# Kernel optimization log

Hardware: AMD Instinct MI355X
Metric: run time of the kernel (lower is better)

Reference implementation:

```python
import jax, jax.numpy as jnp
import numpy as np

DIM = 1024
DEPTH = 2
D_STATE = 16
EXPAND = 2            # standard Mamba expand factor -> d_inner = 2*dim
D_CONV = 4
DT_RANK = DIM // 16   # ceil(dim/16) = 64
D_INNER = DIM * EXPAND
BATCH = 2
SEQ = 1024


def setup_inputs() -> dict:
    key = jax.random.key(0)
    ks = jax.random.split(key, 8)
    def n(k, shape, scale):
        return jax.random.normal(k, shape, jnp.float32) * scale
    # A_log initialized as log(1..N) per channel (S4D-real init, as in mamba_ssm)
    A_log = jnp.tile(jnp.log(jnp.arange(1, D_STATE + 1, dtype=jnp.float32))[None, None, :],
                     (DEPTH, D_INNER, 1))
    return {
        "x": n(ks[0], (BATCH, SEQ, DIM), 1.0),
        "in_proj_w": n(ks[1], (DEPTH, 2 * D_INNER, DIM), DIM ** -0.5),
        "conv_w": n(ks[2], (DEPTH, D_INNER, D_CONV), D_CONV ** -0.5),
        "conv_b": jnp.zeros((DEPTH, D_INNER), jnp.float32),
        "x_proj_w": n(ks[3], (DEPTH, DT_RANK + 2 * D_STATE, D_INNER), D_INNER ** -0.5),
        "dt_proj_w": n(ks[4], (DEPTH, D_INNER, DT_RANK), DT_RANK ** -0.5),
        "dt_proj_b": n(ks[5], (DEPTH, D_INNER), 0.1),
        "A_log": A_log,
        "D": jnp.ones((DEPTH, D_INNER), jnp.float32),
        "out_proj_w": n(ks[6], (DEPTH, DIM, D_INNER), D_INNER ** -0.5),
    }


def _mamba_layer(x, in_w, cw, cb, xp_w, dtw, dtb, A_log, Dp, ow):
    # x: [B, L, dim]
    Bsz = x.shape[0]
    xz = jnp.einsum('bld,ed->ble', x, in_w)            # [B, L, 2*d_inner]
    xi, z = jnp.split(xz, 2, axis=-1)
    # causal depthwise conv1d over time
    xc = jnp.transpose(xi, (0, 2, 1))                  # [B, d_inner, L]
    xc = jax.lax.conv_general_dilated(xc, cw[:, None, :], (1,), [(D_CONV - 1, 0)],
                                      feature_group_count=D_INNER)
    xc = xc + cb[None, :, None]
    xc = jax.nn.silu(jnp.transpose(xc, (0, 2, 1)))     # [B, L, d_inner]
    # input-dependent dt, B, C
    x_dbl = jnp.einsum('bld,ed->ble', xc, xp_w)        # [B, L, dt_rank+2*N]
    dt_raw = x_dbl[..., :DT_RANK]
    Bm = x_dbl[..., DT_RANK:DT_RANK + D_STATE]         # [B, L, N]
    Cm = x_dbl[..., DT_RANK + D_STATE:]                # [B, L, N]
    dt = jax.nn.softplus(jnp.einsum('blr,dr->bld', dt_raw, dtw) + dtb)  # [B, L, d_inner]
    A = -jnp.exp(A_log)                                # [d_inner, N]
    dA = jnp.exp(dt[..., None] * A[None, None])        # [B, L, d_inner, N]
    dBu = dt[..., None] * Bm[:, :, None, :] * xc[..., None]

    def step(h, inp):
        dA_t, dBu_t, C_t = inp
        h = dA_t * h + dBu_t                           # [B, d_inner, N]
        y = jnp.einsum('bdn,bn->bd', h, C_t)
        return h, y

    h0 = jnp.zeros((Bsz, D_INNER, D_STATE), x.dtype)
    _, ys = jax.lax.scan(step, h0,
                         (dA.transpose(1, 0, 2, 3), dBu.transpose(1, 0, 2, 3),
                          Cm.transpose(1, 0, 2)))
    y = ys.transpose(1, 0, 2) + Dp[None, None, :] * xc
    y = y * jax.nn.silu(z)
    return jnp.einsum('bld,od->blo', y, ow)


def reference(x, in_proj_w, conv_w, conv_b, x_proj_w, dt_proj_w, dt_proj_b, A_log, D, out_proj_w):
    for i in range(DEPTH):
        x = _mamba_layer(x, in_proj_w[i], conv_w[i], conv_b[i], x_proj_w[i],
                         dt_proj_w[i], dt_proj_b[i], A_log[i], D[i], out_proj_w[i])
    return x
```

## Files before the change

### kernel.cpp

```cpp
#include <hip/hip_runtime.h>
#include <hip/hip_bf16.h>

typedef __hip_bfloat16 bf16;
typedef __attribute__((ext_vector_type(8))) short short8;
typedef __attribute__((ext_vector_type(4))) short shortx4;
typedef __attribute__((ext_vector_type(4))) float floatx4;

#define BATCH   2
#define SEQ     1024
#define DIM     1024
#define D_INNER 2048
#define D_STATE 16
#define DT_RANK 64
#define MROWS   (BATCH * SEQ)
#define CHUNK   32
#define NCHUNK  (SEQ / CHUNK)

__device__ __forceinline__ float bf2f(bf16 x) { return __bfloat162float(x); }
__device__ __forceinline__ bf16  f2bf(float x) { return __float2bfloat16(x); }
__device__ __forceinline__ short bfbits(float x) {
    bf16 b = __float2bfloat16(x); short s; __builtin_memcpy(&s, &b, 2); return s;
}

__device__ __forceinline__ void ld_lds16(const void* g, void* l) {
    __builtin_amdgcn_global_load_lds(
        (const __attribute__((address_space(1))) void*)g,
        (__attribute__((address_space(3))) void*)l, 16, 0, 0);
}

__device__ __forceinline__ void cast4(const float* in, short* o, int i) {
    floatx4 v = ((const floatx4*)in)[i];
    shortx4 r;
    r.x = bfbits(v.x); r.y = bfbits(v.y); r.z = bfbits(v.z); r.w = bfbits(v.w);
    ((shortx4*)o)[i] = r;
}
__global__ __launch_bounds__(256) void cast_k(
    const float* __restrict__ in, short* __restrict__ o, int n4)
{
    int i = blockIdx.x * 256 + threadIdx.x;
    if (i < n4) cast4(in, o, i);
}
__global__ __launch_bounds__(256) void cast2_k(
    const float* __restrict__ a, short* __restrict__ oa, int na4,
    const float* __restrict__ b, short* __restrict__ ob, int nb4)
{
    int i = blockIdx.x * 256 + threadIdx.x;
    if (i < na4) cast4(a, oa, i);
    else if (i - na4 < nb4) cast4(b, ob, i - na4);
}

__device__ __forceinline__ short8 ld8_any(const void* p, size_t eoff, int is_f32) {
    if (is_f32) {
        const float* f = (const float*)p + eoff;
        floatx4 a = *(const floatx4*)f;
        floatx4 b = *(const floatx4*)(f + 4);
        short8 r;
        r[0] = bfbits(a[0]); r[1] = bfbits(a[1]); r[2] = bfbits(a[2]); r[3] = bfbits(a[3]);
        r[4] = bfbits(b[0]); r[5] = bfbits(b[1]); r[6] = bfbits(b[2]); r[7] = bfbits(b[3]);
        return r;
    } else {
        return *(const short8*)((const bf16*)p + eoff);
    }
}

__global__ __launch_bounds__(256) void gemm128(
    const bf16* __restrict__ A, int lda,
    const bf16* __restrict__ B, int ldb,
    float* __restrict__ Cf, bf16* __restrict__ Cb, int ldc,
    int kchunk, size_t psize)
{
    __shared__ short As[4][128 * 32];
    __shared__ short Bs[4][128 * 32];
    const int tid  = threadIdx.x;
    const int wave = tid >> 6;
    const int lane = tid & 63;
    const int m0 = blockIdx.y * 128;
    const int n0 = blockIdx.x * 128;
    const int wm = (wave & 1) * 64;
    const int wn = (wave >> 1) * 64;
    const int r16  = lane & 15;
    const int quad = lane >> 4;
    const int r0   = tid >> 2;
    const int csw   = (((tid & 3) ^ ((r0 >> 1) & 3)) << 3);
    const int swoff = ((quad ^ ((r16 >> 1) & 3)) << 3);
    const int kbeg = blockIdx.z * kchunk;
    const int nk   = kchunk >> 5;

    floatx4 acc[4][4] = {};

    auto STAGE = [&](int buf, int kk) {
        ld_lds16(A + (size_t)(m0 + r0) * lda + kk + csw,      &As[buf][tid * 8]);
        ld_lds16(A + (size_t)(m0 + r0 + 64) * lda + kk + csw, &As[buf][(tid + 256) * 8]);
        ld_lds16(B + (size_t)(n0 + r0) * ldb + kk + csw,      &Bs[buf][tid * 8]);
        ld_lds16(B + (size_t)(n0 + r0 + 64) * ldb + kk + csw, &Bs[buf][(tid + 256) * 8]);
    };
    auto COMPUTE = [&](int buf) {
        const short* Ab = As[buf];
        const short* Bb = Bs[buf];
        short8 af[4], bg[4];
#pragma unroll
        for (int i = 0; i < 4; i++) {
            af[i] = *(const short8*)(Ab + (wm + i * 16 + r16) * 32 + swoff);
            bg[i] = *(const short8*)(Bb + (wn + i * 16 + r16) * 32 + swoff);
        }
        __builtin_amdgcn_s_setprio(1);
#pragma unroll
        for (int i = 0; i < 4; i++)
#pragma unroll
            for (int j = 0; j < 4; j++)
                acc[i][j] = __builtin_amdgcn_mfma_f32_16x16x32_bf16(af[i], bg[j], acc[i][j], 0, 0, 0);
        __builtin_amdgcn_s_setprio(0);
    };

    STAGE(0, kbeg);
    STAGE(1, kbeg + 32);
    int it = 0;
    for (; it < nk - 2; ++it) {
        STAGE((it + 2) & 3, kbeg + (it + 2) * 32);
        asm volatile("s_waitcnt vmcnt(8) lgkmcnt(0)" ::: "memory");
        __builtin_amdgcn_s_barrier();
        __builtin_amdgcn_sched_barrier(0);
        COMPUTE(it & 3);
    }
    asm volatile("s_waitcnt vmcnt(4) lgkmcnt(0)" ::: "memory");
    __builtin_amdgcn_s_barrier();
    __builtin_amdgcn_sched_barrier(0);
    COMPUTE(it & 3);
    ++it;
    asm volatile("s_waitcnt vmcnt(0) lgkmcnt(0)" ::: "memory");
    __builtin_amdgcn_s_barrier();
    __builtin_amdgcn_sched_barrier(0);
    COMPUTE(it & 3);

    float* Cfp = Cf ? Cf + (size_t)blockIdx.z * psize : nullptr;
#pragma unroll
    for (int i = 0; i < 4; i++)
#pragma unroll
        for (int j = 0; j < 4; j++) {
            int gm = m0 + wm + i * 16 + quad * 4;
            int gn = n0 + wn + j * 16 + r16;
#pragma unroll
            for (int r = 0; r < 4; r++) {
                size_t o = (size_t)(gm + r) * ldc + gn;
                float v = acc[i][j][r];
                if (Cfp) Cfp[o] = v;
                if (Cb) Cb[o] = f2bf(v);
            }
        }
}

__global__ __launch_bounds__(256) void gemm_bt(
    const void* __restrict__ A, int a_f32, int lda,
    const void* __restrict__ B, int b_f32, int ldb,
    float* __restrict__ Cf, bf16* __restrict__ Cb, int ldc,
    int N, int K, size_t psize,
    const float* __restrict__ bias, int act)
{
    __shared__ short As[64][40];
    __shared__ short Bs[64][40];
    const int m0   = blockIdx.y * 64;
    const int n0   = blockIdx.x * 64;
    const int tid  = threadIdx.x;
    const int wave = tid >> 6;
    const int lane = tid & 63;
    const int srow = tid >> 2;
    const int scol = (tid & 3) << 3;
    const int r16  = lane & 15;
    const int quad = lane >> 4;
    const int kbeg = blockIdx.z * K;

    floatx4 acc[4] = {};

    for (int k0 = kbeg; k0 < kbeg + K; k0 += 32) {
        short8 av = ld8_any(A, (size_t)(m0 + srow) * lda + k0 + scol, a_f32);
        short8 bv = {};
        int gn = n0 + srow;
        if (gn < N) bv = ld8_any(B, (size_t)gn * ldb + k0 + scol, b_f32);
        *(short8*)(&As[srow][scol]) = av;
        *(short8*)(&Bs[srow][scol]) = bv;
        __syncthreads();
        short8 af = *(const short8*)(&As[wave * 16 + r16][quad * 8]);
#pragma unroll
        for (int nt = 0; nt < 4; nt++) {
            short8 bq = *(const short8*)(&Bs[nt * 16 + r16][quad * 8]);
            acc[nt] = __builtin_amdgcn_mfma_f32_16x16x32_bf16(af, bq, acc[nt], 0, 0, 0);
        }
        __syncthreads();
    }

    float* Cfp = Cf ? Cf + (size_t)blockIdx.z * psize : nullptr;
#pragma unroll
    for (int nt = 0; nt < 4; nt++) {
        int gn = n0 + nt * 16 + r16;
        if (gn >= N) continue;
        float bsv = bias ? bias[gn] : 0.f;
#pragma unroll
        for (int r = 0; r < 4; r++) {
            int gm = m0 + wave * 16 + quad * 4 + r;
            float v = acc[nt][r] + bsv;
            if (act == 1) v = (v > 20.f) ? v : log1pf(__expf(v));
            size_t o = (size_t)gm * ldc + gn;
            if (Cfp) Cfp[o] = v;
            if (Cb) Cb[o] = f2bf(v);
        }
    }
}

__global__ __launch_bounds__(256) void reduceN_k(
    const float* __restrict__ part, size_t psize, int n, int np,
    float* __restrict__ of, bf16* __restrict__ ob)
{
    int i = blockIdx.x * 256 + threadIdx.x;
    if (i >= n) return;
    float v = 0.f;
    for (int j = 0; j < np; j++) v += part[i + (size_t)j * psize];
    if (of) of[i] = v;
    if (ob) ob[i] = f2bf(v);
}

__global__ __launch_bounds__(256) void conv_silu_k(
    const bf16* __restrict__ xz, const float* __restrict__ cw,
    const float* __restrict__ cb, bf16* __restrict__ xcb)
{
    int idx = blockIdx.x * 256 + threadIdx.x;
    int d   = idx & (D_INNER - 1);
    int bt  = idx >> 11;
    int t   = bt & (SEQ - 1);
    float s = cb[d];
#pragma unroll
    for (int j = 0; j < 4; j++) {
        int tt = t - 3 + j;
        if (tt >= 0) s += cw[d * 4 + j] * bf2f(xz[(size_t)(bt - 3 + j) * 4096 + d]);
    }
    float sig = 1.f / (1.f + __expf(-s));
    xcb[idx] = f2bf(s * sig);
}

__global__ __launch_bounds__(256) void scan1_k(
    const float* __restrict__ dtf, const bf16* __restrict__ xcb,
    const float* __restrict__ xdbl, const float* __restrict__ Alog,
    float* __restrict__ chunk_sdt, float* __restrict__ chunk_S)
{
    __shared__ float dt_s[CHUNK][256];
    __shared__ short xc_s[CHUNK][256];
    __shared__ float B_s[CHUNK][16];
    const int tid = threadIdx.x;
    const int d0  = blockIdx.x * 256;
    const int d   = d0 + tid;
    const int b   = blockIdx.y;
    const int c   = blockIdx.z;
    const size_t rbase = (size_t)b * SEQ + c * CHUNK;

#pragma unroll 4
    for (int t = 0; t < CHUNK; t++) {
        dt_s[t][tid] = dtf[(rbase + t) * D_INNER + d0 + tid];
        ((short*)xc_s)[t * 256 + tid] = *(const short*)&xcb[(rbase + t) * D_INNER + d0 + tid];
    }
    for (int e = tid; e < CHUNK * 16; e += 256) {
        int t = e >> 4, n = e & 15;
        B_s[t][n] = xdbl[(rbase + t) * 96 + 64 + n];
    }
    float A[16];
#pragma unroll
    for (int n = 0; n < 16; n++) A[n] = -__expf(Alog[(size_t)d * 16 + n]);
    float h[16] = {};
    float sdt = 0.f;
    __syncthreads();

    for (int t = 0; t < CHUNK; t++) {
        float dtv = dt_s[t][tid];
        bf16 xcr; short xs = xc_s[t][tid]; __builtin_memcpy(&xcr, &xs, 2);
        float u = dtv * bf2f(xcr);
        sdt += dtv;
        floatx4 B0 = *(const floatx4*)&B_s[t][0];
        floatx4 B1 = *(const floatx4*)&B_s[t][4];
        floatx4 B2 = *(const floatx4*)&B_s[t][8];
        floatx4 B3 = *(const floatx4*)&B_s[t][12];
#pragma unroll
        for (int n = 0; n < 4; n++) {
            h[n]      = __expf(dtv * A[n])      * h[n]      + u * B0[n];
            h[n + 4]  = __expf(dtv * A[n + 4])  * h[n + 4]  + u * B1[n];
            h[n + 8]  = __expf(dtv * A[n + 8])  * h[n + 8]  + u * B2[n];
            h[n + 12] = __expf(dtv * A[n + 12]) * h[n + 12] + u * B3[n];
        }
    }
    chunk_sdt[(b * NCHUNK + c) * D_INNER + d] = sdt;
#pragma unroll
    for (int n = 0; n < 16; n++)
        chunk_S[((size_t)(b * NCHUNK + c) * 16 + n) * D_INNER + d] = h[n];
}

__global__ __launch_bounds__(256) void scanpre_k(
    const float* __restrict__ Alog, const float* __restrict__ chunk_sdt,
    float* __restrict__ chunk_S)
{
    const int d = blockIdx.x * 256 + threadIdx.x;
    const int b = blockIdx.y;
    const int n = blockIdx.z;
    const float Av = -__expf(Alog[(size_t)d * 16 + n]);
    float h = 0.f;
    for (int j = 0; j < NCHUNK; j++) {
        size_t si = ((size_t)(b * NCHUNK + j) * 16 + n) * D_INNER + d;
        float S   = chunk_S[si];
        float sdt = chunk_sdt[(b * NCHUNK + j) * D_INNER + d];
        chunk_S[si] = h;
        h = __expf(sdt * Av) * h + S;
    }
}

__global__ __launch_bounds__(256) void scan2_k(
    const float* __restrict__ dtf, const bf16* __restrict__ xcb,
    const float* __restrict__ xdbl, const bf16* __restrict__ xz,
    const float* __restrict__ Alog, const float* __restrict__ Dp,
    const float* __restrict__ chunk_S, bf16* __restrict__ yb)
{
    __shared__ float dt_s[CHUNK][256];
    __shared__ short xc_s[CHUNK][256];
    __shared__ float B_s[CHUNK][16];
    __shared__ float C_s[CHUNK][16];
    const int tid = threadIdx.x;
    const int d0  = blockIdx.x * 256;
    const int d   = d0 + tid;
    const int b   = blockIdx.y;
    const int c   = blockIdx.z;
    const size_t rbase = (size_t)b * SEQ + c * CHUNK;

#pragma unroll 4
    for (int t = 0; t < CHUNK; t++) {
        dt_s[t][tid] = dtf[(rbase + t) * D_INNER + d0 + tid];
        ((short*)xc_s)[t * 256 + tid] = *(const short*)&xcb[(rbase + t) * D_INNER + d0 + tid];
    }
    for (int e = tid; e < CHUNK * 16; e += 256) {
        int t = e >> 4, n = e & 15;
        B_s[t][n] = xdbl[(rbase + t) * 96 + 64 + n];
        C_s[t][n] = xdbl[(rbase + t) * 96 + 80 + n];
    }
    float A[16];
#pragma unroll
    for (int n = 0; n < 16; n++) A[n] = -__expf(Alog[(size_t)d * 16 + n]);

    float h[16];
#pragma unroll
    for (int n = 0; n < 16; n++)
        h[n] = chunk_S[((size_t)(b * NCHUNK + c) * 16 + n) * D_INNER + d];

    const float Dv = Dp[d];
    __syncthreads();

    for (int t = 0; t < CHUNK; t++) {
        size_t row = rbase + t;
        float dtv = dt_s[t][tid];
        bf16 xcr; short xs = xc_s[t][tid]; __builtin_memcpy(&xcr, &xs, 2);
        float xcv = bf2f(xcr);
        float u = dtv * xcv;
        floatx4 B0 = *(const floatx4*)&B_s[t][0];
        floatx4 B1 = *(const floatx4*)&B_s[t][4];
        floatx4 B2 = *(const floatx4*)&B_s[t][8];
        floatx4 B3 = *(const floatx4*)&B_s[t][12];
        floatx4 C0 = *(const floatx4*)&C_s[t][0];
        floatx4 C1 = *(const floatx4*)&C_s[t][4];
        floatx4 C2 = *(const floatx4*)&C_s[t][8];
        floatx4 C3 = *(const floatx4*)&C_s[t][12];
        float y = 0.f;
#pragma unroll
        for (int n = 0; n < 4; n++) {
            h[n]      = __expf(dtv * A[n])      * h[n]      + u * B0[n];
            h[n + 4]  = __expf(dtv * A[n + 4])  * h[n + 4]  + u * B1[n];
            h[n + 8]  = __expf(dtv * A[n + 8])  * h[n + 8]  + u * B2[n];
            h[n + 12] = __expf(dtv * A[n + 12]) * h[n + 12] + u * B3[n];
            y += h[n] * C0[n] + h[n + 4] * C1[n] + h[n + 8] * C2[n] + h[n + 12] * C3[n];
        }
        float zv = bf2f(xz[row * 4096 + 2048 + d]);
        y = (y + Dv * xcv) * (zv / (1.f + __expf(-zv)));
        yb[row * D_INNER + d] = f2bf(y);
    }
}

extern "C" void kernel_launch(void* const* d_in, const int* in_sizes, int n_in,
                              void* d_out, int out_size, void* d_ws, size_t ws_size,
                              hipStream_t stream)
{
    const float* x    = (const float*)d_in[0];
    const float* inw  = (const float*)d_in[1];
    const float* cw   = (const float*)d_in[2];
    const float* cb   = (const float*)d_in[3];
    const float* xpw  = (const float*)d_in[4];
    const float* dtw  = (const float*)d_in[5];
    const float* dtb  = (const float*)d_in[6];
    const float* Alog = (const float*)d_in[7];
    const float* Dp   = (const float*)d_in[8];
    const float* ow   = (const float*)d_in[9];
    float* out = (float*)d_out;

    char* p = (char*)d_ws;
    bf16*  xzb   = (bf16*)p;  p += (size_t)MROWS * 4096 * 2;
    bf16*  xcb   = (bf16*)p;  p += (size_t)MROWS * D_INNER * 2;
    float* xdblf = (float*)p; p += (size_t)MROWS * 96 * 4;
    float* dtf   = (float*)p; p += (size_t)MROWS * D_INNER * 4;
    bf16*  ybf   = (bf16*)p;  p += (size_t)MROWS * D_INNER * 2;
    bf16*  xmid  = (bf16*)p;  p += (size_t)MROWS * DIM * 2;
    float* csdt  = (float*)p; p += (size_t)BATCH * NCHUNK * D_INNER * 4;
    float* cS    = (float*)p; p += (size_t)BATCH * NCHUNK * 16 * D_INNER * 4;
    bf16*  xb    = (bf16*)p;  p += (size_t)MROWS * DIM * 2;
    bf16*  inwb  = (bf16*)p;  p += (size_t)2 * D_INNER * DIM * 2;
    bf16*  owb   = (bf16*)p;  p += (size_t)DIM * D_INNER * 2;
    float* xprt  = (float*)p; p += (size_t)8 * MROWS * 96 * 4;
    float* oprt  = (float*)p; p += (size_t)4 * MROWS * DIM * 4;

    const size_t xp_psize = (size_t)MROWS * 96;
    const size_t op_psize = (size_t)MROWS * DIM;

    cast_k<<<(MROWS * DIM / 4 + 255) / 256, 256, 0, stream>>>(x, (short*)xb, MROWS * DIM / 4);

    for (int l = 0; l < 2; l++) {
        const float* xpw_l = xpw + (size_t)l * 96 * D_INNER;
        const float* dtw_l = dtw + (size_t)l * D_INNER * DT_RANK;
        const float* Al    = Alog + (size_t)l * D_INNER * D_STATE;

        {
            int na4 = 2 * D_INNER * DIM / 4, nb4 = DIM * D_INNER / 4;
            cast2_k<<<(na4 + nb4 + 255) / 256, 256, 0, stream>>>(
                inw + (size_t)l * 2 * D_INNER * DIM, (short*)inwb, na4,
                ow + (size_t)l * DIM * D_INNER, (short*)owb, nb4);
        }

        gemm128<<<dim3(32, 16, 1), 256, 0, stream>>>(
            (l == 0) ? xb : xmid, DIM, inwb, DIM,
            nullptr, xzb, 4096, DIM, 0);

        conv_silu_k<<<(MROWS * D_INNER) / 256, 256, 0, stream>>>(
            xzb, cw + (size_t)l * D_INNER * 4, cb + (size_t)l * D_INNER, xcb);

        gemm_bt<<<dim3(2, 32, 8), 256, 0, stream>>>(
            xcb, 0, D_INNER, xpw_l, 1, D_INNER,
            xprt, nullptr, 96, 96, 256, xp_psize, nullptr, 0);
        reduceN_k<<<(MROWS * 96 + 255) / 256, 256, 0, stream>>>(
            xprt, xp_psize, MROWS * 96, 8, xdblf, nullptr);

        gemm_bt<<<dim3(32, 32), 256, 0, stream>>>(
            xdblf, 1, 96, dtw_l, 1, DT_RANK,
            dtf, nullptr, D_INNER, D_INNER, DT_RANK, 0,
            dtb + (size_t)l * D_INNER, 1);

        scan1_k<<<dim3(D_INNER / 256, BATCH, NCHUNK), 256, 0, stream>>>(
            dtf, xcb, xdblf, Al, csdt, cS);
        scanpre_k<<<dim3(D_INNER / 256, BATCH, D_STATE), 256, 0, stream>>>(
            Al, csdt, cS);
        scan2_k<<<dim3(D_INNER / 256, BATCH, NCHUNK), 256, 0, stream>>>(
            dtf, xcb, xdblf, xzb, Al, Dp + (size_t)l * D_INNER, cS, ybf);

        gemm128<<<dim3(8, 16, 4), 256, 0, stream>>>(
            ybf, D_INNER, owb, D_INNER,
            oprt, nullptr, DIM, D_INNER / 4, op_psize);
        reduceN_k<<<(MROWS * DIM + 255) / 256, 256, 0, stream>>>(
            oprt, op_psize, MROWS * DIM, 4,
            (l == 1) ? out : nullptr, (l == 0) ? xmid : nullptr);
    }
}
```

Baseline: 422.7 us.

## Batch weight casts, double-buffer gemm_bt loads, vectorize conv_silu

Merges the input cast and both layers' weight casts into one kernel launched once, removing the two per-layer cast launches at the cost of a larger bf16 weight workspace. gemm_bt gets double-buffered LDS with register prefetch of the next K tile, dropping one barrier per iteration so global loads can overlap the MFMAs. conv_silu now has each thread handle 8 channels with 16-byte vector loads and stores, cutting thread count and the number of memory transactions.

```diff
diff --git a/kernel.cpp b/kernel.cpp
--- a/kernel.cpp
+++ b/kernel.cpp
@@ -21,6 +21,9 @@
 __device__ __forceinline__ short bfbits(float x) {
     bf16 b = __float2bfloat16(x); short s; __builtin_memcpy(&s, &b, 2); return s;
 }
+__device__ __forceinline__ float bits2f(short s) {
+    bf16 b; __builtin_memcpy(&b, &s, 2); return __bfloat162float(b);
+}
 
 __device__ __forceinline__ void ld_lds16(const void* g, void* l) {
     __builtin_amdgcn_global_load_lds(
@@ -34,19 +37,15 @@
     r.x = bfbits(v.x); r.y = bfbits(v.y); r.z = bfbits(v.z); r.w = bfbits(v.w);
     ((shortx4*)o)[i] = r;
 }
-__global__ __launch_bounds__(256) void cast_k(
-    const float* __restrict__ in, short* __restrict__ o, int n4)
-{
-    int i = blockIdx.x * 256 + threadIdx.x;
-    if (i < n4) cast4(in, o, i);
-}
-__global__ __launch_bounds__(256) void cast2_k(
+__global__ __launch_bounds__(256) void cast3_k(
     const float* __restrict__ a, short* __restrict__ oa, int na4,
-    const float* __restrict__ b, short* __restrict__ ob, int nb4)
+    const float* __restrict__ b, short* __restrict__ ob, int nb4,
+    const float* __restrict__ c, short* __restrict__ oc, int nc4)
 {
     int i = blockIdx.x * 256 + threadIdx.x;
     if (i < na4) cast4(a, oa, i);
     else if (i - na4 < nb4) cast4(b, ob, i - na4);
+    else if (i - na4 - nb4 < nc4) cast4(c, oc, i - na4 - nb4);
 }
 
 __device__ __forceinline__ short8 ld8_any(const void* p, size_t eoff, int is_f32) {
@@ -156,8 +155,8 @@
     int N, int K, size_t psize,
     const float* __restrict__ bias, int act)
 {
-    __shared__ short As[64][40];
-    __shared__ short Bs[64][40];
+    __shared__ short As[2][64][40];
+    __shared__ short Bs[2][64][40];
     const int m0   = blockIdx.y * 64;
     const int n0   = blockIdx.x * 64;
     const int tid  = threadIdx.x;
@@ -168,24 +167,32 @@
     const int r16  = lane & 15;
     const int quad = lane >> 4;
     const int kbeg = blockIdx.z * K;
+    const int nst  = K >> 5;
+    const int gn_b = n0 + srow;
+    const bool bok = (gn_b < N);
 
     floatx4 acc[4] = {};
 
-    for (int k0 = kbeg; k0 < kbeg + K; k0 += 32) {
-        short8 av = ld8_any(A, (size_t)(m0 + srow) * lda + k0 + scol, a_f32);
-        short8 bv = {};
-        int gn = n0 + srow;
-        if (gn < N) bv = ld8_any(B, (size_t)gn * ldb + k0 + scol, b_f32);
-        *(short8*)(&As[srow][scol]) = av;
-        *(short8*)(&Bs[srow][scol]) = bv;
+    short8 av = ld8_any(A, (size_t)(m0 + srow) * lda + kbeg + scol, a_f32);
+    short8 bv = {};
+    if (bok) bv = ld8_any(B, (size_t)gn_b * ldb + kbeg + scol, b_f32);
+
+    for (int s = 0; s < nst; ++s) {
+        const int cur = s & 1;
+        *(short8*)(&As[cur][srow][scol]) = av;
+        *(short8*)(&Bs[cur][srow][scol]) = bv;
         __syncthreads();
-        short8 af = *(const short8*)(&As[wave * 16 + r16][quad * 8]);
+        if (s + 1 < nst) {
+            int k1 = kbeg + (s + 1) * 32;
+            av = ld8_any(A, (size_t)(m0 + srow) * lda + k1 + scol, a_f32);
+            if (bok) bv = ld8_any(B, (size_t)gn_b * ldb + k1 + scol, b_f32);
+        }
+        short8 af = *(const short8*)(&As[cur][wave * 16 + r16][quad * 8]);
 #pragma unroll
         for (int nt = 0; nt < 4; nt++) {
-            short8 bq = *(const short8*)(&Bs[nt * 16 + r16][quad * 8]);
+            short8 bq = *(const short8*)(&Bs[cur][nt * 16 + r16][quad * 8]);
             acc[nt] = __builtin_amdgcn_mfma_f32_16x16x32_bf16(af, bq, acc[nt], 0, 0, 0);
         }
-        __syncthreads();
     }
 
     float* Cfp = Cf ? Cf + (size_t)blockIdx.z * psize : nullptr;
@@ -223,17 +230,36 @@
     const float* __restrict__ cb, bf16* __restrict__ xcb)
 {
     int idx = blockIdx.x * 256 + threadIdx.x;
-    int d   = idx & (D_INNER - 1);
-    int bt  = idx >> 11;
+    int d   = (idx & 255) << 3;
+    int bt  = idx >> 8;
     int t   = bt & (SEQ - 1);
-    float s = cb[d];
+
+    float s[8];
+    floatx4 cb0 = *(const floatx4*)(cb + d);
+    floatx4 cb1 = *(const floatx4*)(cb + d + 4);
+#pragma unroll
+    for (int i = 0; i < 4; i++) { s[i] = cb0[i]; s[i + 4] = cb1[i]; }
+
+    floatx4 w[8];
+#pragma unroll
+    for (int i = 0; i < 8; i++) w[i] = *(const floatx4*)(cw + (d + i) * 4);
+
 #pragma unroll
     for (int j = 0; j < 4; j++) {
         int tt = t - 3 + j;
-        if (tt >= 0) s += cw[d * 4 + j] * bf2f(xz[(size_t)(bt - 3 + j) * 4096 + d]);
-    }
-    float sig = 1.f / (1.f + __expf(-s));
-    xcb[idx] = f2bf(s * sig);
+        if (tt >= 0) {
+            short8 v = *(const short8*)&xz[(size_t)(bt - 3 + j) * 4096 + d];
+#pragma unroll
+            for (int i = 0; i < 8; i++) s[i] += w[i][j] * bits2f(v[i]);
+        }
+    }
+    short8 r;
+#pragma unroll
+    for (int i = 0; i < 8; i++) {
+        float sig = 1.f / (1.f + __expf(-s[i]));
+        r[i] = bfbits(s[i] * sig);
+    }
+    *(short8*)&xcb[(size_t)bt * D_INNER + d] = r;
 }
 
 __global__ __launch_bounds__(256) void scan1_k(
@@ -269,8 +295,7 @@
 
     for (int t = 0; t < CHUNK; t++) {
         float dtv = dt_s[t][tid];
-        bf16 xcr; short xs = xc_s[t][tid]; __builtin_memcpy(&xcr, &xs, 2);
-        float u = dtv * bf2f(xcr);
+        float u = dtv * bits2f(xc_s[t][tid]);
         sdt += dtv;
         floatx4 B0 = *(const floatx4*)&B_s[t][0];
         floatx4 B1 = *(const floatx4*)&B_s[t][4];
@@ -350,8 +375,7 @@
     for (int t = 0; t < CHUNK; t++) {
         size_t row = rbase + t;
         float dtv = dt_s[t][tid];
-        bf16 xcr; short xs = xc_s[t][tid]; __builtin_memcpy(&xcr, &xs, 2);
-        float xcv = bf2f(xcr);
+        float xcv = bits2f(xc_s[t][tid]);
         float u = dtv * xcv;
         floatx4 B0 = *(const floatx4*)&B_s[t][0];
         floatx4 B1 = *(const floatx4*)&B_s[t][4];
@@ -402,33 +426,34 @@
     float* csdt  = (float*)p; p += (size_t)BATCH * NCHUNK * D_INNER * 4;
     float* cS    = (float*)p; p += (size_t)BATCH * NCHUNK * 16 * D_INNER * 4;
     bf16*  xb    = (bf16*)p;  p += (size_t)MROWS * DIM * 2;
-    bf16*  inwb  = (bf16*)p;  p += (size_t)2 * D_INNER * DIM * 2;
-    bf16*  owb   = (bf16*)p;  p += (size_t)DIM * D_INNER * 2;
+    bf16*  inwb  = (bf16*)p;  p += (size_t)2 * 2 * D_INNER * DIM * 2;
+    bf16*  owb   = (bf16*)p;  p += (size_t)2 * DIM * D_INNER * 2;
     float* xprt  = (float*)p; p += (size_t)8 * MROWS * 96 * 4;
     float* oprt  = (float*)p; p += (size_t)4 * MROWS * DIM * 4;
 
     const size_t xp_psize = (size_t)MROWS * 96;
     const size_t op_psize = (size_t)MROWS * DIM;
 
-    cast_k<<<(MROWS * DIM / 4 + 255) / 256, 256, 0, stream>>>(x, (short*)xb, MROWS * DIM / 4);
+    {
+        int na4 = MROWS * DIM / 4;
+        int nb4 = 2 * 2 * D_INNER * DIM / 4;
+        int nc4 = 2 * DIM * D_INNER / 4;
+        cast3_k<<<(na4 + nb4 + nc4 + 255) / 256, 256, 0, stream>>>(
+            x, (short*)xb, na4, inw, (short*)inwb, nb4, ow, (short*)owb, nc4);
+    }
 
     for (int l = 0; l < 2; l++) {
         const float* xpw_l = xpw + (size_t)l * 96 * D_INNER;
         const float* dtw_l = dtw + (size_t)l * D_INNER * DT_RANK;
         const float* Al    = Alog + (size_t)l * D_INNER * D_STATE;
-
-        {
-            int na4 = 2 * D_INNER * DIM / 4, nb4 = DIM * D_INNER / 4;
-            cast2_k<<<(na4 + nb4 + 255) / 256, 256, 0, stream>>>(
-                inw + (size_t)l * 2 * D_INNER * DIM, (short*)inwb, na4,
-                ow + (size_t)l * DIM * D_INNER, (short*)owb, nb4);
-        }
+        bf16* inwb_l = inwb + (size_t)l * 2 * D_INNER * DIM;
+        bf16* owb_l  = owb  + (size_t)l * DIM * D_INNER;
 
         gemm128<<<dim3(32, 16, 1), 256, 0, stream>>>(
-            (l == 0) ? xb : xmid, DIM, inwb, DIM,
+            (l == 0) ? xb : xmid, DIM, inwb_l, DIM,
             nullptr, xzb, 4096, DIM, 0);
 
-        conv_silu_k<<<(MROWS * D_INNER) / 256, 256, 0, stream>>>(
+        conv_silu_k<<<(MROWS * D_INNER / 8) / 256, 256, 0, stream>>>(
             xzb, cw + (size_t)l * D_INNER * 4, cb + (size_t)l * D_INNER, xcb);
 
         gemm_bt<<<dim3(2, 32, 8), 256, 0, stream>>>(
@@ -450,7 +475,7 @@
             dtf, xcb, xdblf, xzb, Al, Dp + (size_t)l * D_INNER, cS, ybf);
 
         gemm128<<<dim3(8, 16, 4), 256, 0, stream>>>(
-            ybf, D_INNER, owb, D_INNER,
+            ybf, D_INNER, owb_l, D_INNER,
             oprt, nullptr, DIM, D_INNER / 4, op_psize);
         reduceN_k<<<(MROWS * DIM + 255) / 256, 256, 0, stream>>>(
             oprt, op_psize, MROWS * DIM, 4,
```

Result: faster. 403.2 us (-4.6%).
